# Optimization experiments

Measured on AMD Instinct MI355X. Metric: run time of the kernel, lower is better.

Reference implementation:

```python
import jax, jax.numpy as jnp
import numpy as np

E, TOPK = 32, 2            # hardcoded in LossMOEDecoder
D, HID, BOT, OUT = 768, 2048, 256, 768
B, S = 2, 128


def setup_inputs() -> dict:
    key = jax.random.key(0)
    ks = jax.random.split(key, 7)
    p = lambda k, shape: jax.random.normal(k, shape, dtype=jnp.float32) * 0.02
    return {
        "x": jax.random.normal(ks[0], (B, S, D), dtype=jnp.float32),
        "gate_w": p(ks[1], (E, D)),                 # MoEGate.weight
        "W1": p(ks[2], (E, D, HID)),  "b1": jnp.zeros((E, HID), jnp.float32),
        "W2": p(ks[3], (E, HID, HID)), "b2": jnp.zeros((E, HID), jnp.float32),
        "W3": p(ks[4], (E, HID, BOT)), "b3": jnp.zeros((E, BOT), jnp.float32),
        "Wl": p(ks[5], (E, BOT, OUT)), "bl": jnp.zeros((E, OUT), jnp.float32),
    }


def reference(x, gate_w, W1, b1, W2, b2, W3, b3, Wl, bl):
    Bz, Sl, d = x.shape
    xt = x.reshape(-1, d)                                    # [N, d] tokens
    # --- gate: softmax then top-k (values permutation-invariant vs torch sorted=False)
    scores = jax.nn.softmax(xt @ gate_w.T, axis=-1)          # [N, E]
    topk_w, topk_idx = jax.lax.top_k(scores, TOPK)           # [N, k]
    topk_w = topk_w / (topk_w.sum(-1, keepdims=True) + 1e-20)  # norm_topk_prob
    # --- experts: batched over the (small, fixed) expert axis; exact GELU as nn.GELU
    gelu = lambda v: jax.nn.gelu(v, approximate=False)
    h = gelu(jnp.einsum('nd,edh->enh', xt, W1) + b1[:, None, :])   # [E, N, HID]
    h = gelu(jnp.einsum('enh,ehg->eng', h, W2) + b2[:, None, :])   # [E, N, HID]
    z = jnp.einsum('eng,egb->enb', h, W3) + b3[:, None, :]         # [E, N, BOT]
    out_all = jnp.einsum('enb,ebo->eno', z, Wl) + bl[:, None, :]   # [E, N, OUT]
    # --- combine: gather each token's top-k expert outputs, weighted sum
    sel = jnp.take_along_axis(out_all.transpose(1, 0, 2),          # [N, E, OUT]
                              topk_idx[:, :, None], axis=1)        # [N, k, OUT]
    y = (sel * topk_w[:, :, None]).sum(axis=1)                     # [N, OUT]
    return y.reshape(Bz, Sl, OUT)
```

## Files before the change

### kernel.cpp

```cpp
#include <hip/hip_runtime.h>
#include <math.h>

#define NEXP 32
#define NTOK 256
#define DIMD 768
#define DHID 2048
#define DBOT 256
#define DOUT 768
#define NSLOT 512

__global__ __launch_bounds__(64) void gate_kernel(
    const float* __restrict__ x, const float* __restrict__ gw,
    const float* __restrict__ bl, float* __restrict__ y,
    int* __restrict__ topk_idx, float* __restrict__ topk_w,
    float* __restrict__ z) {
  const int n = blockIdx.x;
  const int l = threadIdx.x;
  {
    float4 zv = {0.f, 0.f, 0.f, 0.f};
    float4* zp = (float4*)(z + n * 512 + l * 8);
    zp[0] = zv; zp[1] = zv;
  }
  const float* xr = x + n * DIMD;
  float xs[12];
#pragma unroll
  for (int j = 0; j < 12; j++) xs[j] = xr[l + 64 * j];
  float logit[NEXP];
#pragma unroll
  for (int e = 0; e < NEXP; e++) {
    const float* g = gw + e * DIMD;
    float p = 0.f;
#pragma unroll
    for (int j = 0; j < 12; j++) p = fmaf(xs[j], g[l + 64 * j], p);
#pragma unroll
    for (int m = 1; m < 64; m <<= 1) p += __shfl_xor(p, m);
    logit[e] = p;
  }
  int i0 = 0; float m0 = logit[0];
#pragma unroll
  for (int e = 1; e < NEXP; e++) { if (logit[e] > m0) { m0 = logit[e]; i0 = e; } }
  int i1 = -1; float m1 = -3.4e38f;
#pragma unroll
  for (int e = 0; e < NEXP; e++) { if (e != i0 && logit[e] > m1) { m1 = logit[e]; i1 = e; } }
  const float e1 = expf(m1 - m0);
  const float w0 = 1.f / (1.f + e1);
  const float w1 = e1 * w0;
  if (l == 0) {
    topk_idx[2 * n] = i0; topk_idx[2 * n + 1] = i1;
    topk_w[2 * n] = w0;  topk_w[2 * n + 1] = w1;
  }
  const float* bl0 = bl + i0 * DOUT;
  const float* bl1 = bl + i1 * DOUT;
#pragma unroll
  for (int j = 0; j < 12; j++) {
    const int o = l + 64 * j;
    y[n * DOUT + o] = fmaf(w0, bl0[o], w1 * bl1[o]);
  }
}

__global__ __launch_bounds__(256) void build_lists(
    const int* __restrict__ topk_idx, const float* __restrict__ topk_w,
    int* __restrict__ counts, int* __restrict__ offsets,
    int* __restrict__ tok_list, float* __restrict__ tok_wt) {
  __shared__ int cnt[NEXP], base[NEXP], fill[NEXP];
  const int t = threadIdx.x;
  if (t < NEXP) { cnt[t] = 0; fill[t] = 0; }
  __syncthreads();
  const int e0 = topk_idx[2 * t], e1 = topk_idx[2 * t + 1];
  atomicAdd(&cnt[e0], 1);
  atomicAdd(&cnt[e1], 1);
  __syncthreads();
  if (t == 0) { int s = 0; for (int i = 0; i < NEXP; i++) { base[i] = s; s += cnt[i]; } }
  __syncthreads();
  const int p0 = atomicAdd(&fill[e0], 1);
  tok_list[base[e0] + p0] = t; tok_wt[base[e0] + p0] = topk_w[2 * t];
  const int p1 = atomicAdd(&fill[e1], 1);
  tok_list[base[e1] + p1] = t; tok_wt[base[e1] + p1] = topk_w[2 * t + 1];
  if (t < NEXP) { counts[t] = cnt[t]; offsets[t] = base[t]; }
}

__device__ __forceinline__ float gelu_f(float v) {
  return 0.5f * v * (1.f + erff(v * 0.70710678118654752f));
}

template <int MODE>
__global__ __launch_bounds__(1024) void ff_kernel(
    const float* __restrict__ Ain, const float* __restrict__ W,
    const float* __restrict__ Bias, float* __restrict__ Out,
    const int* __restrict__ offsets, const int* __restrict__ counts,
    const int* __restrict__ tok_list, const float* __restrict__ tok_wt,
    int KTOT, int NCT, int INS, int kblocks, int coltiles) {
  __shared__ float lds[32768];
  const int tid  = threadIdx.x;
  const int lane = tid & 63;
  const int wave = tid >> 6;
  const int cg   = wave & 1;
  const int ks   = wave >> 1;
  const int e    = blockIdx.y;
  const int ct   = blockIdx.x % coltiles;
  const int kb   = blockIdx.x / coltiles;
  const int KB   = KTOT / kblocks;
  const int cnt  = counts[e];
  const int off  = offsets[e];
  const int cb   = ct * 256;
  const float* Wblk = W + ((size_t)e * KTOT + (size_t)kb * KB) * NCT + cb;
  const int wcol = cg * 128 + lane;

  for (int tc0 = 0; tc0 < cnt; tc0 += 32) {
    const int tcn = min(32, cnt - tc0);
    float acc[2][32];
#pragma unroll
    for (int c = 0; c < 2; c++)
#pragma unroll
      for (int t = 0; t < 32; t++) acc[c][t] = 0.f;

    for (int sb = 0; sb < KB; sb += 512) {
      const int sec = min(512, KB - sb);
      __syncthreads();
      {
        const int t  = tid >> 5;
        const int per = sec >> 5;
        const int r0 = (tid & 31) * per;
        if (t < tcn) {
          const int slot = off + tc0 + t;
          const float* src;
          if (MODE == 0) src = Ain + (size_t)tok_list[slot] * INS + kb * KB + sb + r0;
          else           src = Ain + (size_t)slot * INS + kb * KB + sb + r0;
          float* dst = &lds[t * sec + r0];
          for (int j = 0; j < per; j += 4) {
            float4 v = *(const float4*)(src + j);
            if (MODE == 3) {
              const float4 bv = *(const float4*)(Bias + e * KTOT + sb + r0 + j);
              v.x += bv.x; v.y += bv.y; v.z += bv.z; v.w += bv.w;
            }
            *(float4*)(dst + j) = v;
          }
        }
      }
      __syncthreads();
      const int srows = sec >> 3;
      const int rs = ks * srows;
      for (int g = 0; g < srows; g += 4) {
        float w0[4], w1[4];
        const float* wp = Wblk + (size_t)(sb + rs + g) * NCT + wcol;
#pragma unroll
        for (int j = 0; j < 4; j++) {
          w0[j] = wp[(size_t)j * NCT];
          w1[j] = wp[(size_t)j * NCT + 64];
        }
#pragma unroll
        for (int t = 0; t < 32; t++) {
          const float4 xv = *(const float4*)&lds[t * sec + rs + g];
          acc[0][t] = fmaf(xv.x, w0[0], acc[0][t]);
          acc[0][t] = fmaf(xv.y, w0[1], acc[0][t]);
          acc[0][t] = fmaf(xv.z, w0[2], acc[0][t]);
          acc[0][t] = fmaf(xv.w, w0[3], acc[0][t]);
          acc[1][t] = fmaf(xv.x, w1[0], acc[1][t]);
          acc[1][t] = fmaf(xv.y, w1[1], acc[1][t]);
          acc[1][t] = fmaf(xv.z, w1[2], acc[1][t]);
          acc[1][t] = fmaf(xv.w, w1[3], acc[1][t]);
        }
      }
    }
#pragma unroll
    for (int c = 0; c < 2; c++) {
      __syncthreads();
#pragma unroll
      for (int t = 0; t < 32; t++) lds[t * 1024 + tid] = acc[c][t];
      __syncthreads();
      const int p  = tid & 127;
      const int t0 = (tid >> 7) << 2;
      for (int i = 0; i < 4; i++) {
        const int t = t0 + i;
        if (t >= tcn) break;
        float s = 0.f;
#pragma unroll
        for (int k2 = 0; k2 < 8; k2++) s += lds[t * 1024 + k2 * 128 + p];
        const int col  = cb + (p >> 6) * 128 + c * 64 + (p & 63);
        const int slot = off + tc0 + t;
        if (MODE <= 1) {
          Out[(size_t)slot * NCT + col] = gelu_f(s + Bias[e * NCT + col]);
        } else if (MODE == 2) {
          atomicAdd(&Out[(size_t)slot * NCT + col], s);
        } else {
          atomicAdd(&Out[(size_t)tok_list[slot] * NCT + col], tok_wt[slot] * s);
        }
      }
    }
  }
}

extern "C" void kernel_launch(void* const* d_in, const int* in_sizes, int n_in,
                              void* d_out, int out_size, void* d_ws, size_t ws_size,
                              hipStream_t stream) {
  const float* x  = (const float*)d_in[0];
  const float* gw = (const float*)d_in[1];
  const float* W1 = (const float*)d_in[2];
  const float* b1 = (const float*)d_in[3];
  const float* W2 = (const float*)d_in[4];
  const float* b2 = (const float*)d_in[5];
  const float* W3 = (const float*)d_in[6];
  const float* b3 = (const float*)d_in[7];
  const float* Wl = (const float*)d_in[8];
  const float* bl = (const float*)d_in[9];
  float* y  = (float*)d_out;
  float* ws = (float*)d_ws;

  float* topk_w   = ws;
  int*   topk_idx = (int*)(ws + 512);
  int*   counts   = (int*)(ws + 1024);
  int*   offsets  = (int*)(ws + 1056);
  int*   tok_list = (int*)(ws + 1088);
  float* tok_wt   = ws + 1600;
  float* h1 = ws + 4096;
  float* h2 = h1 + (size_t)NSLOT * DHID;
  float* z  = h2 + (size_t)NSLOT * DHID;

  gate_kernel<<<NTOK, 64, 0, stream>>>(x, gw, bl, y, topk_idx, topk_w, z);
  build_lists<<<1, 256, 0, stream>>>(topk_idx, topk_w, counts, offsets, tok_list, tok_wt);
  ff_kernel<0><<<dim3(8, 32), 1024, 0, stream>>>(x,  W1, b1, h1, offsets, counts, tok_list, tok_wt,
                                                 DIMD, DHID, DIMD, 1, 8);
  ff_kernel<1><<<dim3(8, 32), 1024, 0, stream>>>(h1, W2, b2, h2, offsets, counts, tok_list, tok_wt,
                                                 DHID, DHID, DHID, 1, 8);
  ff_kernel<2><<<dim3(8, 32), 1024, 0, stream>>>(h2, W3, nullptr, z, offsets, counts, tok_list, tok_wt,
                                                 DHID, DBOT, DHID, 8, 1);
  ff_kernel<3><<<dim3(3, 32), 1024, 0, stream>>>(z,  Wl, b3, y, offsets, counts, tok_list, tok_wt,
                                                 DBOT, DOUT, DBOT, 1, 3);
}
```

Baseline: 421.1 us.

## Double-buffer LDS activation staging with async global_load_lds and float2 weight loads

Restructures the expert FF kernel so activation sections are staged into two alternating LDS buffers, loading the next section while the current one is computed. Non-MODE-3 staging uses the global_load_lds builtin to copy directly from global to LDS, with zero-fill for padded token rows. Each lane now loads float2 weights for adjacent columns and prefetches the next row group in registers, and the output path writes float2 results. These changes aim to hide global memory latency and halve the number of weight load instructions, at the cost of more registers and LDS traffic complexity.

```diff
diff --git a/kernel.cpp b/kernel.cpp
--- a/kernel.cpp
+++ b/kernel.cpp
@@ -81,6 +81,44 @@
 
 __device__ __forceinline__ float gelu_f(float v) {
   return 0.5f * v * (1.f + erff(v * 0.70710678118654752f));
+}
+
+template <int SEC>
+__device__ __forceinline__ void compute_sec(
+    const float* __restrict__ buf, const float* __restrict__ Wseg, int NCT,
+    float* acc0, float* acc1, int ks) {
+  const int srows = SEC >> 3;
+  const int rs = ks * srows;
+  const float* wp = Wseg + (size_t)rs * NCT;
+  float2 wa[4];
+#pragma unroll
+  for (int j = 0; j < 4; j++) wa[j] = *(const float2*)(wp + (size_t)j * NCT);
+  for (int g = 0; g < srows; g += 4) {
+    float2 wb[4];
+    const bool more = (g + 4 < srows);
+    if (more) {
+      const float* wn = wp + (size_t)(g + 4) * NCT;
+#pragma unroll
+      for (int j = 0; j < 4; j++) wb[j] = *(const float2*)(wn + (size_t)j * NCT);
+    }
+    const float* bp = buf + rs + g;
+#pragma unroll
+    for (int t = 0; t < 32; t++) {
+      const float4 xv = *(const float4*)(bp + t * SEC);
+      acc0[t] = fmaf(xv.x, wa[0].x, acc0[t]);
+      acc1[t] = fmaf(xv.x, wa[0].y, acc1[t]);
+      acc0[t] = fmaf(xv.y, wa[1].x, acc0[t]);
+      acc1[t] = fmaf(xv.y, wa[1].y, acc1[t]);
+      acc0[t] = fmaf(xv.z, wa[2].x, acc0[t]);
+      acc1[t] = fmaf(xv.z, wa[2].y, acc1[t]);
+      acc0[t] = fmaf(xv.w, wa[3].x, acc0[t]);
+      acc1[t] = fmaf(xv.w, wa[3].y, acc1[t]);
+    }
+    if (more) {
+#pragma unroll
+      for (int j = 0; j < 4; j++) wa[j] = wb[j];
+    }
+  }
 }
 
 template <int MODE>
@@ -104,89 +142,127 @@
   const int off  = offsets[e];
   const int cb   = ct * 256;
   const float* Wblk = W + ((size_t)e * KTOT + (size_t)kb * KB) * NCT + cb;
-  const int wcol = cg * 128 + lane;
+  const int wcol2 = cg * 128 + 2 * lane;
+  const int nsec = (KB + 511) >> 9;
 
   for (int tc0 = 0; tc0 < cnt; tc0 += 32) {
     const int tcn = min(32, cnt - tc0);
-    float acc[2][32];
-#pragma unroll
-    for (int c = 0; c < 2; c++)
-#pragma unroll
-      for (int t = 0; t < 32; t++) acc[c][t] = 0.f;
-
-    for (int sb = 0; sb < KB; sb += 512) {
+    float acc0[32], acc1[32];
+#pragma unroll
+    for (int t = 0; t < 32; t++) { acc0[t] = 0.f; acc1[t] = 0.f; }
+
+    const float* rowb[2];
+#pragma unroll
+    for (int i = 0; i < 2; i++) {
+      const int slot = off + tc0 + 2 * wave + i;
+      const int srow = (MODE == 0) ? tok_list[min(slot, NSLOT - 1)]
+                                   : min(slot, NSLOT - 1);
+      rowb[i] = Ain + (size_t)srow * INS + (size_t)kb * KB;
+    }
+
+    auto stage = [&](int b, int s) {
+      const int sb  = s << 9;
       const int sec = min(512, KB - sb);
-      __syncthreads();
-      {
+      float* bufp = lds + b * 16384;
+      if (MODE == 3) {
         const int t  = tid >> 5;
-        const int per = sec >> 5;
-        const int r0 = (tid & 31) * per;
+        const int r0 = (tid & 31) * 8;
+        float* dst = bufp + t * sec + r0;
         if (t < tcn) {
           const int slot = off + tc0 + t;
-          const float* src;
-          if (MODE == 0) src = Ain + (size_t)tok_list[slot] * INS + kb * KB + sb + r0;
-          else           src = Ain + (size_t)slot * INS + kb * KB + sb + r0;
-          float* dst = &lds[t * sec + r0];
-          for (int j = 0; j < per; j += 4) {
+          const float* src = Ain + (size_t)slot * INS + sb + r0;
+          const float* bsrc = Bias + e * KTOT + sb + r0;
+#pragma unroll
+          for (int j = 0; j < 8; j += 4) {
             float4 v = *(const float4*)(src + j);
-            if (MODE == 3) {
-              const float4 bv = *(const float4*)(Bias + e * KTOT + sb + r0 + j);
-              v.x += bv.x; v.y += bv.y; v.z += bv.z; v.w += bv.w;
+            const float4 bv = *(const float4*)(bsrc + j);
+            v.x += bv.x; v.y += bv.y; v.z += bv.z; v.w += bv.w;
+            *(float4*)(dst + j) = v;
+          }
+        } else {
+          const float4 zz = {0.f, 0.f, 0.f, 0.f};
+#pragma unroll
+          for (int j = 0; j < 8; j += 4) *(float4*)(dst + j) = zz;
+        }
+      } else {
+#pragma unroll
+        for (int i = 0; i < 2; i++) {
+          const int t = 2 * wave + i;
+          float* ldst = bufp + t * sec;
+          if (t < tcn) {
+            const float* row = rowb[i] + sb;
+            for (int c = 0; c < sec; c += 256) {
+              __builtin_amdgcn_global_load_lds(
+                  (const __attribute__((address_space(1))) void*)(row + c + lane * 4),
+                  (__attribute__((address_space(3))) void*)(ldst + c),
+                  16, 0, 0);
             }
-            *(float4*)(dst + j) = v;
+          } else {
+            const float4 zz = {0.f, 0.f, 0.f, 0.f};
+            for (int c = 0; c < sec; c += 256)
+              *(float4*)(ldst + c + lane * 4) = zz;
           }
         }
       }
+    };
+
+    stage(0, 0);
+    __syncthreads();
+    for (int s = 0; s < nsec; s++) {
+      if (s + 1 < nsec) stage((s + 1) & 1, s + 1);
+      const int sb  = s << 9;
+      const int sec = min(512, KB - sb);
+      const float* bufp = lds + (s & 1) * 16384;
+      const float* Wseg = Wblk + (size_t)sb * NCT + wcol2;
+      if (sec == 512) compute_sec<512>(bufp, Wseg, NCT, acc0, acc1, ks);
+      else            compute_sec<256>(bufp, Wseg, NCT, acc0, acc1, ks);
       __syncthreads();
-      const int srows = sec >> 3;
-      const int rs = ks * srows;
-      for (int g = 0; g < srows; g += 4) {
-        float w0[4], w1[4];
-        const float* wp = Wblk + (size_t)(sb + rs + g) * NCT + wcol;
-#pragma unroll
-        for (int j = 0; j < 4; j++) {
-          w0[j] = wp[(size_t)j * NCT];
-          w1[j] = wp[(size_t)j * NCT + 64];
-        }
-#pragma unroll
-        for (int t = 0; t < 32; t++) {
-          const float4 xv = *(const float4*)&lds[t * sec + rs + g];
-          acc[0][t] = fmaf(xv.x, w0[0], acc[0][t]);
-          acc[0][t] = fmaf(xv.y, w0[1], acc[0][t]);
-          acc[0][t] = fmaf(xv.z, w0[2], acc[0][t]);
-          acc[0][t] = fmaf(xv.w, w0[3], acc[0][t]);
-          acc[1][t] = fmaf(xv.x, w1[0], acc[1][t]);
-          acc[1][t] = fmaf(xv.y, w1[1], acc[1][t]);
-          acc[1][t] = fmaf(xv.z, w1[2], acc[1][t]);
-          acc[1][t] = fmaf(xv.w, w1[3], acc[1][t]);
+    }
+
+    const int p  = tid & 127;
+    const int t0 = (tid >> 7) << 2;
+    const int colbase = cb + (p >> 6) * 128 + 2 * (p & 63);
+    float sv[4];
+#pragma unroll
+    for (int t = 0; t < 32; t++) lds[t * 1024 + tid] = acc0[t];
+    __syncthreads();
+#pragma unroll
+    for (int i = 0; i < 4; i++) {
+      float s = 0.f;
+#pragma unroll
+      for (int k2 = 0; k2 < 8; k2++) s += lds[(t0 + i) * 1024 + k2 * 128 + p];
+      sv[i] = s;
+    }
+    __syncthreads();
+#pragma unroll
+    for (int t = 0; t < 32; t++) lds[t * 1024 + tid] = acc1[t];
+    __syncthreads();
+#pragma unroll
+    for (int i = 0; i < 4; i++) {
+      const int t = t0 + i;
+      if (t < tcn) {
+        float s1 = 0.f;
+#pragma unroll
+        for (int k2 = 0; k2 < 8; k2++) s1 += lds[t * 1024 + k2 * 128 + p];
+        const int slot = off + tc0 + t;
+        if (MODE <= 1) {
+          const float2 bv = *(const float2*)(Bias + e * NCT + colbase);
+          float2 o;
+          o.x = gelu_f(sv[i] + bv.x);
+          o.y = gelu_f(s1 + bv.y);
+          *(float2*)(Out + (size_t)slot * NCT + colbase) = o;
+        } else if (MODE == 2) {
+          atomicAdd(&Out[(size_t)slot * NCT + colbase], sv[i]);
+          atomicAdd(&Out[(size_t)slot * NCT + colbase + 1], s1);
+        } else {
+          const int trow = tok_list[slot];
+          const float wgt = tok_wt[slot];
+          atomicAdd(&Out[(size_t)trow * NCT + colbase], wgt * sv[i]);
+          atomicAdd(&Out[(size_t)trow * NCT + colbase + 1], wgt * s1);
         }
       }
     }
-#pragma unroll
-    for (int c = 0; c < 2; c++) {
-      __syncthreads();
-#pragma unroll
-      for (int t = 0; t < 32; t++) lds[t * 1024 + tid] = acc[c][t];
-      __syncthreads();
-      const int p  = tid & 127;
-      const int t0 = (tid >> 7) << 2;
-      for (int i = 0; i < 4; i++) {
-        const int t = t0 + i;
-        if (t >= tcn) break;
-        float s = 0.f;
-#pragma unroll
-        for (int k2 = 0; k2 < 8; k2++) s += lds[t * 1024 + k2 * 128 + p];
-        const int col  = cb + (p >> 6) * 128 + c * 64 + (p & 63);
-        const int slot = off + tc0 + t;
-        if (MODE <= 1) {
-          Out[(size_t)slot * NCT + col] = gelu_f(s + Bias[e * NCT + col]);
-        } else if (MODE == 2) {
-          atomicAdd(&Out[(size_t)slot * NCT + col], s);
-        } else {
-          atomicAdd(&Out[(size_t)tok_list[slot] * NCT + col], tok_wt[slot] * s);
-        }
-      }
-    }
+    __syncthreads();
   }
 }
 
```

Result: slower. 702.1 us (+66.7%).

## Double-buffer expert activations via direct global-to-LDS loads with prefetched weights

Applied to the files above, without the earlier changes.

Rewrites the expert FFN kernel to use 512 threads with two K-halves, each wave computing 64 columns for 32 tokens. Activations are staged into double-buffered LDS through global_load_lds, so the load of the next section overlaps compute on the current one. Weight rows are software-prefetched two groups ahead. The cross-wave reduction shrinks to a single pairwise sum. The last layer is also split over two K-blocks to raise block count. The cost is more blocks per expert and added complexity in the staging index math.

```diff
diff --git a/kernel.cpp b/kernel.cpp
--- a/kernel.cpp
+++ b/kernel.cpp
@@ -83,110 +83,139 @@
   return 0.5f * v * (1.f + erff(v * 0.70710678118654752f));
 }
 
+template <int SEC>
+__device__ __forceinline__ void compute_sec(
+    const float* __restrict__ buf, const float* __restrict__ wp, int NCT,
+    float* acc) {
+  constexpr int ngg = SEC >> 2;
+  float wr[2][4];
+#pragma unroll
+  for (int d = 0; d < 2; d++)
+#pragma unroll
+    for (int j = 0; j < 4; j++) wr[d][j] = wp[(size_t)(4 * d + j) * NCT];
+#pragma unroll 2
+  for (int gg = 0; gg < ngg; ++gg) {
+    const int d = gg & 1;
+    const float* bp = buf + 4 * gg;
+#pragma unroll
+    for (int t = 0; t < 32; t++) {
+      const float4 xv = *(const float4*)(bp + t * SEC);
+      acc[t] = fmaf(xv.x, wr[d][0], acc[t]);
+      acc[t] = fmaf(xv.y, wr[d][1], acc[t]);
+      acc[t] = fmaf(xv.z, wr[d][2], acc[t]);
+      acc[t] = fmaf(xv.w, wr[d][3], acc[t]);
+    }
+    const int gp = min(gg + 2, ngg - 1);
+#pragma unroll
+    for (int j = 0; j < 4; j++) wr[d][j] = wp[(size_t)(4 * gp + j) * NCT];
+  }
+}
+
 template <int MODE>
-__global__ __launch_bounds__(1024) void ff_kernel(
+__global__ __launch_bounds__(512) void ff_kernel(
     const float* __restrict__ Ain, const float* __restrict__ W,
     const float* __restrict__ Bias, float* __restrict__ Out,
     const int* __restrict__ offsets, const int* __restrict__ counts,
     const int* __restrict__ tok_list, const float* __restrict__ tok_wt,
     int KTOT, int NCT, int INS, int kblocks, int coltiles) {
-  __shared__ float lds[32768];
+  __shared__ float lds[2][2][32 * 256];
   const int tid  = threadIdx.x;
   const int lane = tid & 63;
   const int wave = tid >> 6;
-  const int cg   = wave & 1;
-  const int ks   = wave >> 1;
+  const int cg   = wave & 3;
+  const int h    = wave >> 2;
   const int e    = blockIdx.y;
   const int ct   = blockIdx.x % coltiles;
   const int kb   = blockIdx.x / coltiles;
   const int KB   = KTOT / kblocks;
+  const int HK   = KB >> 1;
+  const int nsec = (HK + 255) >> 8;
   const int cnt  = counts[e];
   const int off  = offsets[e];
   const int cb   = ct * 256;
+  const int wcol = cg * 64 + lane;
   const float* Wblk = W + ((size_t)e * KTOT + (size_t)kb * KB) * NCT + cb;
-  const int wcol = cg * 128 + lane;
 
   for (int tc0 = 0; tc0 < cnt; tc0 += 32) {
     const int tcn = min(32, cnt - tc0);
-    float acc[2][32];
-#pragma unroll
-    for (int c = 0; c < 2; c++)
-#pragma unroll
-      for (int t = 0; t < 32; t++) acc[c][t] = 0.f;
-
-    for (int sb = 0; sb < KB; sb += 512) {
-      const int sec = min(512, KB - sb);
-      __syncthreads();
-      {
-        const int t  = tid >> 5;
-        const int per = sec >> 5;
-        const int r0 = (tid & 31) * per;
-        if (t < tcn) {
-          const int slot = off + tc0 + t;
-          const float* src;
-          if (MODE == 0) src = Ain + (size_t)tok_list[slot] * INS + kb * KB + sb + r0;
-          else           src = Ain + (size_t)slot * INS + kb * KB + sb + r0;
-          float* dst = &lds[t * sec + r0];
-          for (int j = 0; j < per; j += 4) {
-            float4 v = *(const float4*)(src + j);
-            if (MODE == 3) {
-              const float4 bv = *(const float4*)(Bias + e * KTOT + sb + r0 + j);
-              v.x += bv.x; v.y += bv.y; v.z += bv.z; v.w += bv.w;
-            }
-            *(float4*)(dst + j) = v;
-          }
+    float acc[32];
+#pragma unroll
+    for (int t = 0; t < 32; t++) acc[t] = 0.f;
+
+    auto stage = [&](int buf, int s) {
+      if (MODE == 3) {
+        const int f   = tid << 3;
+        const int tok = f >> 7;
+        const int k0  = f & 127;
+        const int slot = min(off + tc0 + tok, NSLOT - 1);
+        const float* src  = Ain + (size_t)slot * INS + kb * KB + k0;
+        const float* bsrc = Bias + e * KTOT + kb * KB + k0;
+#pragma unroll
+        for (int i = 0; i < 2; i++) {
+          const int k = k0 + i * 4;
+          float4 v = *(const float4*)(src + i * 4);
+          const float4 bv = *(const float4*)(bsrc + i * 4);
+          v.x += bv.x; v.y += bv.y; v.z += bv.z; v.w += bv.w;
+          *(float4*)(&lds[k >> 6][buf][tok * 64 + (k & 63)]) = v;
+        }
+      } else {
+        const int sec = min(256, HK - (s << 8));
+        const int ls  = 31 - __clz(sec);
+        const int ncalls = (sec << 5) >> 8;
+        float* base = &lds[h][buf][0];
+        const int basecol = kb * KB + h * HK + (s << 8);
+        for (int c = cg; c < ncalls; c += 4) {
+          const int f0  = (c << 8) + lane * 4;
+          const int tok = f0 >> ls;
+          const int k   = f0 & (sec - 1);
+          const int slot = min(off + tc0 + tok, NSLOT - 1);
+          const int row  = (MODE == 0) ? tok_list[slot] : slot;
+          const float* src = Ain + (size_t)row * INS + basecol + k;
+          __builtin_amdgcn_global_load_lds(
+              (const __attribute__((address_space(1))) void*)src,
+              (__attribute__((address_space(3))) void*)(base + (c << 8)),
+              16, 0, 0);
         }
       }
+    };
+
+    stage(0, 0);
+    __syncthreads();
+    int buf = 0;
+    for (int s = 0; s < nsec; s++) {
+      if (s + 1 < nsec) stage(buf ^ 1, s + 1);
+      const int sec = min(256, HK - (s << 8));
+      const float* bufp = &lds[h][buf][0];
+      const float* wp = Wblk + (size_t)(h * HK + (s << 8)) * NCT + wcol;
+      if (sec == 256)      compute_sec<256>(bufp, wp, NCT, acc);
+      else if (sec == 128) compute_sec<128>(bufp, wp, NCT, acc);
+      else                 compute_sec<64>(bufp, wp, NCT, acc);
       __syncthreads();
-      const int srows = sec >> 3;
-      const int rs = ks * srows;
-      for (int g = 0; g < srows; g += 4) {
-        float w0[4], w1[4];
-        const float* wp = Wblk + (size_t)(sb + rs + g) * NCT + wcol;
-#pragma unroll
-        for (int j = 0; j < 4; j++) {
-          w0[j] = wp[(size_t)j * NCT];
-          w1[j] = wp[(size_t)j * NCT + 64];
-        }
-#pragma unroll
-        for (int t = 0; t < 32; t++) {
-          const float4 xv = *(const float4*)&lds[t * sec + rs + g];
-          acc[0][t] = fmaf(xv.x, w0[0], acc[0][t]);
-          acc[0][t] = fmaf(xv.y, w0[1], acc[0][t]);
-          acc[0][t] = fmaf(xv.z, w0[2], acc[0][t]);
-          acc[0][t] = fmaf(xv.w, w0[3], acc[0][t]);
-          acc[1][t] = fmaf(xv.x, w1[0], acc[1][t]);
-          acc[1][t] = fmaf(xv.y, w1[1], acc[1][t]);
-          acc[1][t] = fmaf(xv.z, w1[2], acc[1][t]);
-          acc[1][t] = fmaf(xv.w, w1[3], acc[1][t]);
+      buf ^= 1;
+    }
+
+    float* red = &lds[0][0][0];
+    if (h == 1) {
+#pragma unroll
+      for (int t = 0; t < 32; t++) red[t * 256 + wcol] = acc[t];
+    }
+    __syncthreads();
+    if (h == 0) {
+      const int col = cb + wcol;
+      const float bcol = (MODE <= 1) ? Bias[e * NCT + col] : 0.f;
+      for (int t = 0; t < tcn; t++) {
+        const float s2 = acc[t] + red[t * 256 + wcol];
+        const int slot = off + tc0 + t;
+        if (MODE <= 1) {
+          Out[(size_t)slot * NCT + col] = gelu_f(s2 + bcol);
+        } else if (MODE == 2) {
+          atomicAdd(&Out[(size_t)slot * NCT + col], s2);
+        } else {
+          atomicAdd(&Out[(size_t)tok_list[slot] * NCT + col], tok_wt[slot] * s2);
         }
       }
     }
-#pragma unroll
-    for (int c = 0; c < 2; c++) {
-      __syncthreads();
-#pragma unroll
-      for (int t = 0; t < 32; t++) lds[t * 1024 + tid] = acc[c][t];
-      __syncthreads();
-      const int p  = tid & 127;
-      const int t0 = (tid >> 7) << 2;
-      for (int i = 0; i < 4; i++) {
-        const int t = t0 + i;
-        if (t >= tcn) break;
-        float s = 0.f;
-#pragma unroll
-        for (int k2 = 0; k2 < 8; k2++) s += lds[t * 1024 + k2 * 128 + p];
-        const int col  = cb + (p >> 6) * 128 + c * 64 + (p & 63);
-        const int slot = off + tc0 + t;
-        if (MODE <= 1) {
-          Out[(size_t)slot * NCT + col] = gelu_f(s + Bias[e * NCT + col]);
-        } else if (MODE == 2) {
-          atomicAdd(&Out[(size_t)slot * NCT + col], s);
-        } else {
-          atomicAdd(&Out[(size_t)tok_list[slot] * NCT + col], tok_wt[slot] * s);
-        }
-      }
-    }
+    __syncthreads();
   }
 }
 
@@ -218,12 +247,12 @@
 
   gate_kernel<<<NTOK, 64, 0, stream>>>(x, gw, bl, y, topk_idx, topk_w, z);
   build_lists<<<1, 256, 0, stream>>>(topk_idx, topk_w, counts, offsets, tok_list, tok_wt);
-  ff_kernel<0><<<dim3(8, 32), 1024, 0, stream>>>(x,  W1, b1, h1, offsets, counts, tok_list, tok_wt,
-                                                 DIMD, DHID, DIMD, 1, 8);
-  ff_kernel<1><<<dim3(8, 32), 1024, 0, stream>>>(h1, W2, b2, h2, offsets, counts, tok_list, tok_wt,
-                                                 DHID, DHID, DHID, 1, 8);
-  ff_kernel<2><<<dim3(8, 32), 1024, 0, stream>>>(h2, W3, nullptr, z, offsets, counts, tok_list, tok_wt,
-                                                 DHID, DBOT, DHID, 8, 1);
-  ff_kernel<3><<<dim3(3, 32), 1024, 0, stream>>>(z,  Wl, b3, y, offsets, counts, tok_list, tok_wt,
-                                                 DBOT, DOUT, DBOT, 1, 3);
-}
+  ff_kernel<0><<<dim3(8, 32), 512, 0, stream>>>(x,  W1, b1, h1, offsets, counts, tok_list, tok_wt,
+                                                DIMD, DHID, DIMD, 1, 8);
+  ff_kernel<1><<<dim3(8, 32), 512, 0, stream>>>(h1, W2, b2, h2, offsets, counts, tok_list, tok_wt,
+                                                DHID, DHID, DHID, 1, 8);
+  ff_kernel<2><<<dim3(8, 32), 512, 0, stream>>>(h2, W3, nullptr, z, offsets, counts, tok_list, tok_wt,
+                                                DHID, DBOT, DHID, 8, 1);
+  ff_kernel<3><<<dim3(6, 32), 512, 0, stream>>>(z,  Wl, b3, y, offsets, counts, tok_list, tok_wt,
+                                                DBOT, DOUT, DBOT, 2, 3);
+}
```

New measurement: 543.5 us. +29.1%, slower.

## Split-K MoE expert GEMMs across many small blocks with atomic accumulation and separate GELU pass

Applied to the files above, without the earlier changes.

Replaces the 1024-thread per-expert blocks with 256-thread blocks that each handle a 256-row K slice, so W1 and W2 layers launch 24x32 and 64x32 blocks. Partial sums go into zeroed buffers through atomics, and bias plus GELU move into a separate gelu_pass kernel that also re-zeroes the accumulator. Activations are staged into LDS with global_load_lds, and weight loads are software-prefetched two steps ahead. The aim is better CU occupancy and memory-level parallelism for the weight-bandwidth-bound expert matmuls, at the cost of extra atomics, extra kernels, and more buffer zeroing traffic.

```diff
diff --git a/kernel.cpp b/kernel.cpp
--- a/kernel.cpp
+++ b/kernel.cpp
@@ -8,18 +8,22 @@
 #define DBOT 256
 #define DOUT 768
 #define NSLOT 512
+#define CHUNK 16
 
 __global__ __launch_bounds__(64) void gate_kernel(
     const float* __restrict__ x, const float* __restrict__ gw,
     const float* __restrict__ bl, float* __restrict__ y,
     int* __restrict__ topk_idx, float* __restrict__ topk_w,
-    float* __restrict__ z) {
+    float* __restrict__ z, float* __restrict__ A) {
   const int n = blockIdx.x;
   const int l = threadIdx.x;
   {
-    float4 zv = {0.f, 0.f, 0.f, 0.f};
+    const float4 zv = {0.f, 0.f, 0.f, 0.f};
     float4* zp = (float4*)(z + n * 512 + l * 8);
     zp[0] = zv; zp[1] = zv;
+    float4* ap = (float4*)(A + (size_t)n * 4096 + l * 64);
+#pragma unroll
+    for (int j = 0; j < 16; j++) ap[j] = zv;
   }
   const float* xr = x + n * DIMD;
   float xs[12];
@@ -61,7 +65,8 @@
 __global__ __launch_bounds__(256) void build_lists(
     const int* __restrict__ topk_idx, const float* __restrict__ topk_w,
     int* __restrict__ counts, int* __restrict__ offsets,
-    int* __restrict__ tok_list, float* __restrict__ tok_wt) {
+    int* __restrict__ tok_list, float* __restrict__ tok_wt,
+    int* __restrict__ slot_expert) {
   __shared__ int cnt[NEXP], base[NEXP], fill[NEXP];
   const int t = threadIdx.x;
   if (t < NEXP) { cnt[t] = 0; fill[t] = 0; }
@@ -74,8 +79,10 @@
   __syncthreads();
   const int p0 = atomicAdd(&fill[e0], 1);
   tok_list[base[e0] + p0] = t; tok_wt[base[e0] + p0] = topk_w[2 * t];
+  slot_expert[base[e0] + p0] = e0;
   const int p1 = atomicAdd(&fill[e1], 1);
   tok_list[base[e1] + p1] = t; tok_wt[base[e1] + p1] = topk_w[2 * t + 1];
+  slot_expert[base[e1] + p1] = e1;
   if (t < NEXP) { counts[t] = cnt[t]; offsets[t] = base[t]; }
 }
 
@@ -83,110 +90,141 @@
   return 0.5f * v * (1.f + erff(v * 0.70710678118654752f));
 }
 
+__global__ __launch_bounds__(256) void gelu_pass(
+    const float* __restrict__ A, const float* __restrict__ bias,
+    float* __restrict__ Bout, float* __restrict__ Azero,
+    const int* __restrict__ slot_expert) {
+  const int slot = blockIdx.x;
+  const int e = slot_expert[slot];
+  const int c0 = threadIdx.x * 8;
+  const float* ap = A + (size_t)slot * DHID + c0;
+  const float* bp = bias + (size_t)e * DHID + c0;
+  float* op = Bout + (size_t)slot * DHID + c0;
+  float* zp = Azero + (size_t)slot * DHID + c0;
+  const float4 zz = {0.f, 0.f, 0.f, 0.f};
+#pragma unroll
+  for (int j = 0; j < 8; j += 4) {
+    const float4 a = *(const float4*)(ap + j);
+    const float4 b = *(const float4*)(bp + j);
+    float4 o;
+    o.x = gelu_f(a.x + b.x); o.y = gelu_f(a.y + b.y);
+    o.z = gelu_f(a.z + b.z); o.w = gelu_f(a.w + b.w);
+    *(float4*)(op + j) = o;
+    *(float4*)(zp + j) = zz;
+  }
+}
+
 template <int MODE>
-__global__ __launch_bounds__(1024) void ff_kernel(
+__global__ __launch_bounds__(256) void ff_kernel(
     const float* __restrict__ Ain, const float* __restrict__ W,
     const float* __restrict__ Bias, float* __restrict__ Out,
     const int* __restrict__ offsets, const int* __restrict__ counts,
     const int* __restrict__ tok_list, const float* __restrict__ tok_wt,
-    int KTOT, int NCT, int INS, int kblocks, int coltiles) {
-  __shared__ float lds[32768];
+    int KTOT, int NCT, int INS, int coltiles) {
+  __shared__ float act[CHUNK * 256];
   const int tid  = threadIdx.x;
   const int lane = tid & 63;
   const int wave = tid >> 6;
   const int cg   = wave & 1;
-  const int ks   = wave >> 1;
+  const int kh   = wave >> 1;
   const int e    = blockIdx.y;
   const int ct   = blockIdx.x % coltiles;
   const int kb   = blockIdx.x / coltiles;
-  const int KB   = KTOT / kblocks;
   const int cnt  = counts[e];
   const int off  = offsets[e];
   const int cb   = ct * 256;
-  const float* Wblk = W + ((size_t)e * KTOT + (size_t)kb * KB) * NCT + cb;
-  const int wcol = cg * 128 + lane;
-
-  for (int tc0 = 0; tc0 < cnt; tc0 += 32) {
-    const int tcn = min(32, cnt - tc0);
-    float acc[2][32];
-#pragma unroll
-    for (int c = 0; c < 2; c++)
-#pragma unroll
-      for (int t = 0; t < 32; t++) acc[c][t] = 0.f;
-
-    for (int sb = 0; sb < KB; sb += 512) {
-      const int sec = min(512, KB - sb);
-      __syncthreads();
-      {
-        const int t  = tid >> 5;
-        const int per = sec >> 5;
-        const int r0 = (tid & 31) * per;
-        if (t < tcn) {
-          const int slot = off + tc0 + t;
-          const float* src;
-          if (MODE == 0) src = Ain + (size_t)tok_list[slot] * INS + kb * KB + sb + r0;
-          else           src = Ain + (size_t)slot * INS + kb * KB + sb + r0;
-          float* dst = &lds[t * sec + r0];
-          for (int j = 0; j < per; j += 4) {
-            float4 v = *(const float4*)(src + j);
-            if (MODE == 3) {
-              const float4 bv = *(const float4*)(Bias + e * KTOT + sb + r0 + j);
-              v.x += bv.x; v.y += bv.y; v.z += bv.z; v.w += bv.w;
-            }
-            *(float4*)(dst + j) = v;
-          }
+  const int wcol2 = cg * 128 + 2 * lane;
+  const float* Wblk = W + ((size_t)e * KTOT + (size_t)kb * 256 + kh * 128) * NCT + cb + wcol2;
+
+  for (int tc0 = 0; tc0 < cnt; tc0 += CHUNK) {
+    const int tcn = min(CHUNK, cnt - tc0);
+    if (MODE == 3) {
+      const int t  = tid >> 4;
+      const int r0 = (tid & 15) * 16;
+      const int slot = min(off + tc0 + t, NSLOT - 1);
+      const float* src  = Ain + (size_t)slot * INS + r0;
+      const float* bsrc = Bias + (size_t)e * KTOT + r0;
+      float* dst = act + t * 256 + r0;
+#pragma unroll
+      for (int j = 0; j < 16; j += 4) {
+        float4 v = *(const float4*)(src + j);
+        const float4 bv = *(const float4*)(bsrc + j);
+        v.x += bv.x; v.y += bv.y; v.z += bv.z; v.w += bv.w;
+        *(float4*)(dst + j) = v;
+      }
+    } else {
+#pragma unroll
+      for (int i = 0; i < 4; i++) {
+        const int t = wave * 4 + i;
+        const int slot = min(off + tc0 + t, NSLOT - 1);
+        const int row  = (MODE == 0) ? tok_list[slot] : slot;
+        const float* src = Ain + (size_t)row * INS + (size_t)kb * 256 + lane * 4;
+        __builtin_amdgcn_global_load_lds(
+            (const __attribute__((address_space(1))) void*)src,
+            (__attribute__((address_space(3))) void*)(act + t * 256),
+            16, 0, 0);
+      }
+    }
+    __syncthreads();
+
+    float acc0[CHUNK], acc1[CHUNK];
+#pragma unroll
+    for (int t = 0; t < CHUNK; t++) { acc0[t] = 0.f; acc1[t] = 0.f; }
+    float2 wbuf[4][4];
+#pragma unroll
+    for (int j = 0; j < 4; j++) {
+      wbuf[0][j] = *(const float2*)(Wblk + (size_t)j * NCT);
+      wbuf[1][j] = *(const float2*)(Wblk + (size_t)(4 + j) * NCT);
+    }
+#pragma unroll 4
+    for (int g = 0; g < 32; ++g) {
+      const int cur = g & 3;
+      const int nxt = (g + 2) & 3;
+      const int gp  = min(g + 2, 31);
+      const float* wn = Wblk + (size_t)(4 * gp) * NCT;
+#pragma unroll
+      for (int j = 0; j < 4; j++) wbuf[nxt][j] = *(const float2*)(wn + (size_t)j * NCT);
+      const float* bp = act + kh * 128 + 4 * g;
+#pragma unroll
+      for (int t = 0; t < CHUNK; t++) {
+        const float4 xv = *(const float4*)(bp + t * 256);
+        acc0[t] = fmaf(xv.x, wbuf[cur][0].x, acc0[t]);
+        acc1[t] = fmaf(xv.x, wbuf[cur][0].y, acc1[t]);
+        acc0[t] = fmaf(xv.y, wbuf[cur][1].x, acc0[t]);
+        acc1[t] = fmaf(xv.y, wbuf[cur][1].y, acc1[t]);
+        acc0[t] = fmaf(xv.z, wbuf[cur][2].x, acc0[t]);
+        acc1[t] = fmaf(xv.z, wbuf[cur][2].y, acc1[t]);
+        acc0[t] = fmaf(xv.w, wbuf[cur][3].x, acc0[t]);
+        acc1[t] = fmaf(xv.w, wbuf[cur][3].y, acc1[t]);
+      }
+    }
+
+    __syncthreads();
+    if (kh == 1) {
+#pragma unroll
+      for (int t = 0; t < CHUNK; t++) {
+        act[t * 256 + wcol2]     = acc0[t];
+        act[t * 256 + wcol2 + 1] = acc1[t];
+      }
+    }
+    __syncthreads();
+    if (kh == 0) {
+      for (int t = 0; t < tcn; t++) {
+        const float s0 = acc0[t] + act[t * 256 + wcol2];
+        const float s1 = acc1[t] + act[t * 256 + wcol2 + 1];
+        const int slot = off + tc0 + t;
+        if (MODE <= 2) {
+          atomicAdd(&Out[(size_t)slot * NCT + cb + wcol2], s0);
+          atomicAdd(&Out[(size_t)slot * NCT + cb + wcol2 + 1], s1);
+        } else {
+          const int trow = tok_list[slot];
+          const float wgt = tok_wt[slot];
+          atomicAdd(&Out[(size_t)trow * NCT + cb + wcol2], wgt * s0);
+          atomicAdd(&Out[(size_t)trow * NCT + cb + wcol2 + 1], wgt * s1);
         }
       }
-      __syncthreads();
-      const int srows = sec >> 3;
-      const int rs = ks * srows;
-      for (int g = 0; g < srows; g += 4) {
-        float w0[4], w1[4];
-        const float* wp = Wblk + (size_t)(sb + rs + g) * NCT + wcol;
-#pragma unroll
-        for (int j = 0; j < 4; j++) {
-          w0[j] = wp[(size_t)j * NCT];
-          w1[j] = wp[(size_t)j * NCT + 64];
-        }
-#pragma unroll
-        for (int t = 0; t < 32; t++) {
-          const float4 xv = *(const float4*)&lds[t * sec + rs + g];
-          acc[0][t] = fmaf(xv.x, w0[0], acc[0][t]);
-          acc[0][t] = fmaf(xv.y, w0[1], acc[0][t]);
-          acc[0][t] = fmaf(xv.z, w0[2], acc[0][t]);
-          acc[0][t] = fmaf(xv.w, w0[3], acc[0][t]);
-          acc[1][t] = fmaf(xv.x, w1[0], acc[1][t]);
-          acc[1][t] = fmaf(xv.y, w1[1], acc[1][t]);
-          acc[1][t] = fmaf(xv.z, w1[2], acc[1][t]);
-          acc[1][t] = fmaf(xv.w, w1[3], acc[1][t]);
-        }
-      }
-    }
-#pragma unroll
-    for (int c = 0; c < 2; c++) {
-      __syncthreads();
-#pragma unroll
-      for (int t = 0; t < 32; t++) lds[t * 1024 + tid] = acc[c][t];
-      __syncthreads();
-      const int p  = tid & 127;
-      const int t0 = (tid >> 7) << 2;
-      for (int i = 0; i < 4; i++) {
-        const int t = t0 + i;
-        if (t >= tcn) break;
-        float s = 0.f;
-#pragma unroll
-        for (int k2 = 0; k2 < 8; k2++) s += lds[t * 1024 + k2 * 128 + p];
-        const int col  = cb + (p >> 6) * 128 + c * 64 + (p & 63);
-        const int slot = off + tc0 + t;
-        if (MODE <= 1) {
-          Out[(size_t)slot * NCT + col] = gelu_f(s + Bias[e * NCT + col]);
-        } else if (MODE == 2) {
-          atomicAdd(&Out[(size_t)slot * NCT + col], s);
-        } else {
-          atomicAdd(&Out[(size_t)tok_list[slot] * NCT + col], tok_wt[slot] * s);
-        }
-      }
-    }
+    }
+    __syncthreads();
   }
 }
 
@@ -212,18 +250,21 @@
   int*   offsets  = (int*)(ws + 1056);
   int*   tok_list = (int*)(ws + 1088);
   float* tok_wt   = ws + 1600;
-  float* h1 = ws + 4096;
-  float* h2 = h1 + (size_t)NSLOT * DHID;
-  float* z  = h2 + (size_t)NSLOT * DHID;
-
-  gate_kernel<<<NTOK, 64, 0, stream>>>(x, gw, bl, y, topk_idx, topk_w, z);
-  build_lists<<<1, 256, 0, stream>>>(topk_idx, topk_w, counts, offsets, tok_list, tok_wt);
-  ff_kernel<0><<<dim3(8, 32), 1024, 0, stream>>>(x,  W1, b1, h1, offsets, counts, tok_list, tok_wt,
-                                                 DIMD, DHID, DIMD, 1, 8);
-  ff_kernel<1><<<dim3(8, 32), 1024, 0, stream>>>(h1, W2, b2, h2, offsets, counts, tok_list, tok_wt,
-                                                 DHID, DHID, DHID, 1, 8);
-  ff_kernel<2><<<dim3(8, 32), 1024, 0, stream>>>(h2, W3, nullptr, z, offsets, counts, tok_list, tok_wt,
-                                                 DHID, DBOT, DHID, 8, 1);
-  ff_kernel<3><<<dim3(3, 32), 1024, 0, stream>>>(z,  Wl, b3, y, offsets, counts, tok_list, tok_wt,
-                                                 DBOT, DOUT, DBOT, 1, 3);
-}
+  int*   slot_exp = (int*)(ws + 2112);
+  float* A = ws + 4096;
+  float* B = A + (size_t)NSLOT * DHID;
+  float* z = B + (size_t)NSLOT * DHID;
+
+  gate_kernel<<<NTOK, 64, 0, stream>>>(x, gw, bl, y, topk_idx, topk_w, z, A);
+  build_lists<<<1, 256, 0, stream>>>(topk_idx, topk_w, counts, offsets, tok_list, tok_wt, slot_exp);
+  ff_kernel<0><<<dim3(24, 32), 256, 0, stream>>>(x, W1, nullptr, A, offsets, counts,
+                                                 tok_list, tok_wt, DIMD, DHID, DIMD, 8);
+  gelu_pass<<<NSLOT, 256, 0, stream>>>(A, b1, B, A, slot_exp);
+  ff_kernel<1><<<dim3(64, 32), 256, 0, stream>>>(B, W2, nullptr, A, offsets, counts,
+                                                 tok_list, tok_wt, DHID, DHID, DHID, 8);
+  gelu_pass<<<NSLOT, 256, 0, stream>>>(A, b2, B, A, slot_exp);
+  ff_kernel<2><<<dim3(8, 32), 256, 0, stream>>>(B, W3, nullptr, z, offsets, counts,
+                                                tok_list, tok_wt, DHID, DBOT, DHID, 1);
+  ff_kernel<3><<<dim3(3, 32), 256, 0, stream>>>(z, Wl, b3, y, offsets, counts,
+                                                tok_list, tok_wt, DBOT, DOUT, DBOT, 3);
+}
```

New measurement: 464.2 us. 10.2% more time.
